# Kernel optimization log

Hardware: AMD Instinct MI355X
Metric: run time of the kernel (lower is better)

The kernel has to match this reference:

```python
import jax, jax.numpy as jnp
import numpy as np

N_NODES = 50000
N_EDGES = 800000
DIMS = [100, 512, 256, 128, 200]  # input -> conv1 -> conv2 -> conv3 -> conv4


def setup_inputs() -> dict:
    key = jax.random.key(0)
    ks = jax.random.split(key, 2 + 4)
    x = jax.random.normal(ks[0], (N_NODES, DIMS[0]), dtype=jnp.float32)
    edge_index = jax.random.randint(ks[1], (2, N_EDGES), 0, N_NODES, dtype=jnp.int64)
    inp = {"x": x, "edge_index": edge_index}
    for i in range(4):
        fan_in = DIMS[i]
        W = jax.random.normal(ks[2 + i], (DIMS[i], DIMS[i + 1]), dtype=jnp.float32) * (1.0 / np.sqrt(fan_in)).astype(np.float32)
        b = jnp.zeros((DIMS[i + 1],), dtype=jnp.float32)
        inp[f"W{i + 1}"] = W
        inp[f"b{i + 1}"] = b
    return inp


def _gcn_layer(x, row, col, norm, W, b, n):
    # PyG GCNConv: linear transform first, then normalized scatter-add, then bias.
    h = x @ W                           # [N, out]
    msg = h[row] * norm[:, None]        # [E+N, out] gather + edge scale
    agg = jax.ops.segment_sum(msg, col, num_segments=n)  # scatter-add to targets
    return agg + b


def reference(x, edge_index, W1, b1, W2, b2, W3, b3, W4, b4):
    n = x.shape[0]
    loop = jnp.arange(n, dtype=edge_index.dtype)
    row = jnp.concatenate([edge_index[0], loop])  # sources (with self-loops)
    col = jnp.concatenate([edge_index[1], loop])  # targets (with self-loops)
    deg = jax.ops.segment_sum(jnp.ones_like(col, dtype=x.dtype), col, num_segments=n)
    dinv = jnp.where(deg > 0, jax.lax.rsqrt(deg), 0.0)
    norm = dinv[row] * dinv[col]  # symmetric D^{-1/2}(A+I)D^{-1/2} edge weights

    out = jax.nn.relu(_gcn_layer(x, row, col, norm, W1, b1, n))
    out = jax.nn.relu(_gcn_layer(out, row, col, norm, W2, b2, n))
    out = jax.nn.relu(_gcn_layer(out, row, col, norm, W3, b3, n))
    out = jax.nn.relu(_gcn_layer(out, row, col, norm, W4, b4, n))
    return jnp.mean(out, axis=0, keepdims=True)  # [1, 200]
```

## Files before the change

kernel.cpp:

```cpp
#include <hip/hip_runtime.h>
#include <hip/hip_bf16.h>


#define NN 50000
#define NE 800000
#define NPART 8
#define PRANGE (NN / NPART)

typedef __attribute__((ext_vector_type(8))) _Float16 f16x8;
typedef __attribute__((ext_vector_type(4))) float floatx4;
typedef __attribute__((ext_vector_type(2))) float floatx2;

union U16x8 {
    uint4 u4;
    f16x8 h;
    _Float16 e[8];
};

__device__ __forceinline__ void dec16(const unsigned char* p, float* f) {
    uint4 v = *(const uint4*)p;
    unsigned w[4] = {v.x, v.y, v.z, v.w};
#pragma unroll
    for (int k = 0; k < 4; k++) {
        floatx2 lo = __builtin_amdgcn_cvt_pk_f32_fp8(w[k], false);
        floatx2 hi = __builtin_amdgcn_cvt_pk_f32_fp8(w[k], true);
        f[k * 4 + 0] = lo[0];
        f[k * 4 + 1] = lo[1];
        f[k * 4 + 2] = hi[0];
        f[k * 4 + 3] = hi[1];
    }
}

__device__ __forceinline__ uint4 enc16(const float* f) {
    uint4 r;
    unsigned w;
    w = __builtin_amdgcn_cvt_pk_fp8_f32(f[0], f[1], 0, false);
    w = __builtin_amdgcn_cvt_pk_fp8_f32(f[2], f[3], (int)w, true);
    r.x = w;
    w = __builtin_amdgcn_cvt_pk_fp8_f32(f[4], f[5], 0, false);
    w = __builtin_amdgcn_cvt_pk_fp8_f32(f[6], f[7], (int)w, true);
    r.y = w;
    w = __builtin_amdgcn_cvt_pk_fp8_f32(f[8], f[9], 0, false);
    w = __builtin_amdgcn_cvt_pk_fp8_f32(f[10], f[11], (int)w, true);
    r.z = w;
    w = __builtin_amdgcn_cvt_pk_fp8_f32(f[12], f[13], 0, false);
    w = __builtin_amdgcn_cvt_pk_fp8_f32(f[14], f[15], (int)w, true);
    r.w = w;
    return r;
}

__device__ __forceinline__ uint4 dec8_f16(uint2 v) {
    floatx2 f0 = __builtin_amdgcn_cvt_pk_f32_fp8(v.x, false);
    floatx2 f1 = __builtin_amdgcn_cvt_pk_f32_fp8(v.x, true);
    floatx2 f2 = __builtin_amdgcn_cvt_pk_f32_fp8(v.y, false);
    floatx2 f3 = __builtin_amdgcn_cvt_pk_f32_fp8(v.y, true);
    U16x8 o;
    o.e[0] = (_Float16)f0[0]; o.e[1] = (_Float16)f0[1];
    o.e[2] = (_Float16)f1[0]; o.e[3] = (_Float16)f1[1];
    o.e[4] = (_Float16)f2[0]; o.e[5] = (_Float16)f2[1];
    o.e[6] = (_Float16)f3[0]; o.e[7] = (_Float16)f3[1];
    return o.u4;
}

__global__ __launch_bounds__(256) void zero_detect_kernel(
    const unsigned* __restrict__ ei, int* __restrict__ flag,
    unsigned* __restrict__ cnt, unsigned* __restrict__ fillc,
    float* __restrict__ out) {
    int tid = blockIdx.x * 256 + threadIdx.x;
    if (tid < NN) {
        cnt[tid] = 0u;
        fillc[tid] = 0u;
    }
    if (blockIdx.x == 0) {
        if (threadIdx.x < 200) out[threadIdx.x] = 0.f;
        unsigned w = ei[2 * threadIdx.x + 1];
        unsigned long long any = __ballot(w != 0);
        if (threadIdx.x == 0) *flag = (any == 0ull) ? 1 : 0;
    }
}

__global__ __launch_bounds__(256) void count_kernel(const void* ei,
                                                    const int* __restrict__ flag,
                                                    unsigned* __restrict__ cnt) {
    const int part = blockIdx.x & 7;
    const int lo = part * PRANGE, hi = lo + PRANGE;
    const int group = blockIdx.x >> 3;
    const int f64 = *flag;
    const long long* p64 = (const long long*)ei + NE;
    const int* p32 = (const int*)ei + NE;
    for (int e = group * 256 + threadIdx.x; e < NE; e += 128 * 256) {
        int c = f64 ? (int)p64[e] : p32[e];
        if (c >= lo && c < hi) atomicAdd(&cnt[c], 1u);
    }
}

__global__ __launch_bounds__(256) void scan1_kernel(const unsigned* __restrict__ cnt,
                                                    int* __restrict__ off,
                                                    int* __restrict__ bsum,
                                                    float* __restrict__ dinv) {
    __shared__ int ws[4];
    int b = blockIdx.x, t = threadIdx.x;
    int base = b * 1024 + t * 4;
    int v[4];
    int s = 0;
#pragma unroll
    for (int i = 0; i < 4; i++) {
        int val = 0;
        if (base + i < NN) {
            val = (int)cnt[base + i];
            dinv[base + i] = rsqrtf((float)(val + 1));
        }
        v[i] = s;
        s += val;
    }
    int lane = t & 63, wv = t >> 6;
    int x = s;
    for (int d = 1; d < 64; d <<= 1) {
        int y = __shfl_up(x, d, 64);
        if (lane >= d) x += y;
    }
    if (lane == 63) ws[wv] = x;
    __syncthreads();
    int wpre = 0;
#pragma unroll
    for (int i = 0; i < 4; i++)
        if (i < wv) wpre += ws[i];
    int texcl = x - s + wpre;
#pragma unroll
    for (int i = 0; i < 4; i++)
        if (base + i < NN) off[base + i] = texcl + v[i];
    if (t == 255) bsum[b] = texcl + s;
}

__global__ void scan2_kernel(int* bsum, int nb) {
    int t = threadIdx.x;
    int v = (t < nb) ? bsum[t] : 0;
    int x = v;
    for (int d = 1; d < 64; d <<= 1) {
        int y = __shfl_up(x, d, 64);
        if (t >= d) x += y;
    }
    if (t < nb) bsum[t] = x - v;
}

__global__ __launch_bounds__(256) void scan3_kernel(int* __restrict__ off,
                                                    const int* __restrict__ bsum) {
    int b = blockIdx.x;
    int add = bsum[b];
    int base = b * 1024 + threadIdx.x * 4;
#pragma unroll
    for (int i = 0; i < 4; i++)
        if (base + i < NN) off[base + i] += add;
    if (b == 0 && threadIdx.x == 0) off[NN] = NE;
}

__global__ __launch_bounds__(256) void fill_kernel(
    const void* ei, const int* __restrict__ flag, const int* __restrict__ off,
    unsigned* __restrict__ fillc, int* __restrict__ ep) {
    const int part = blockIdx.x & 7;
    const int lo = part * PRANGE, hi = lo + PRANGE;
    const int group = blockIdx.x >> 3;
    const int f64 = *flag;
    const long long* p64 = (const long long*)ei;
    const int* p32 = (const int*)ei;
    for (int e = group * 256 + threadIdx.x; e < NE; e += 128 * 256) {
        int c = f64 ? (int)p64[NE + e] : p32[NE + e];
        if (c >= lo && c < hi) {
            int r = f64 ? (int)p64[e] : p32[e];
            int pos = off[c] + (int)atomicAdd(&fillc[c], 1u);
            ep[pos] = r;
        }
    }
}

__global__ __launch_bounds__(256) void xwcast_kernel(
    const float* __restrict__ x, unsigned char* __restrict__ xb,
    const float* __restrict__ W1, const float* __restrict__ W2,
    const float* __restrict__ W3, const float* __restrict__ W4,
    _Float16* __restrict__ w1t, _Float16* __restrict__ w2t,
    _Float16* __restrict__ w3t, _Float16* __restrict__ w4t) {
    int bx = blockIdx.x, t = threadIdx.x;
    if (bx < 1563) {
        int tid = bx * 256 + t;
        int node = tid >> 3, sub = tid & 7;
        if (node >= NN) return;
        int base = sub * 16;
        float f[16];
#pragma unroll
        for (int i = 0; i < 16; i++) {
            int c = base + i;
            f[i] = (c < 100) ? x[(size_t)node * 100 + c] : 0.f;
        }
        *(uint4*)(xb + (size_t)node * 128 + base) = enc16(f);
        return;
    }
    int b = bx - 1563;
    const float* W;
    _Float16* Wt;
    int K, N, Kpad, tid;
    if (b < 256)      { W = W1; Wt = w1t; K = 100; N = 512; Kpad = 128; tid = b * 256 + t; }
    else if (b < 768) { W = W2; Wt = w2t; K = 512; N = 256; Kpad = 512; tid = (b - 256) * 256 + t; }
    else if (b < 896) { W = W3; Wt = w3t; K = 256; N = 128; Kpad = 256; tid = (b - 768) * 256 + t; }
    else              { W = W4; Wt = w4t; K = 128; N = 200; Kpad = 128; tid = (b - 896) * 256 + t; }
    int n = tid / Kpad, k = tid - n * Kpad;
    float v = (k < K && n < N) ? W[(size_t)k * N + n] : 0.f;
    Wt[tid] = (_Float16)v;
}

template <int D, int BR>
__global__ __launch_bounds__(256) void agg_kernel(
    const unsigned char* __restrict__ H, const int* __restrict__ off,
    const int* __restrict__ ep, const float* __restrict__ dinv,
    const float* __restrict__ bias, unsigned char* __restrict__ O) {
    constexpr int LPN = D / 16;
    int tid = blockIdx.x * 256 + threadIdx.x;
    int node = tid / LPN;
    int sub = tid % LPN;
    if (node >= NN) return;
    int s = off[node], e = off[node + 1];
    float dc = dinv[node];
    float selfw = dc * dc;
    const int base = sub * 16;
    const unsigned char* __restrict__ Hb = H + base;
    float acc[16], t0[16], t1[16];
    dec16(Hb + (size_t)node * D, t0);
#pragma unroll
    for (int i = 0; i < 16; i++) acc[i] = selfw * t0[i];
    int j = s;
    for (; j + 2 <= e; j += 2) {
        int r0 = ep[j];
        int r1 = ep[j + 1];
        float w0 = dinv[r0] * dc;
        float w1 = dinv[r1] * dc;
        dec16(Hb + (size_t)r0 * D, t0);
        dec16(Hb + (size_t)r1 * D, t1);
#pragma unroll
        for (int i = 0; i < 16; i++) acc[i] = fmaf(w0, t0[i], acc[i]);
#pragma unroll
        for (int i = 0; i < 16; i++) acc[i] = fmaf(w1, t1[i], acc[i]);
    }
    if (j < e) {
        int r0 = ep[j];
        float w0 = dinv[r0] * dc;
        dec16(Hb + (size_t)r0 * D, t0);
#pragma unroll
        for (int i = 0; i < 16; i++) acc[i] = fmaf(w0, t0[i], acc[i]);
    }
    if (BR) {
#pragma unroll
        for (int i = 0; i < 16; i++) acc[i] = fmaxf(acc[i] + bias[base + i], 0.f);
    }
    *(uint4*)(O + (size_t)node * D + base) = enc16(acc);
}

template <int EPI>
__global__ __launch_bounds__(256) void gemm_kernel(
    const unsigned char* __restrict__ A, const _Float16* __restrict__ B,
    const float* __restrict__ bias, unsigned char* __restrict__ Cb,
    float* __restrict__ outmean, int M, int K, int N) {
    __shared__ _Float16 Asl[128 * 40];
    __shared__ _Float16 Bsl[128 * 40];
    __shared__ float red[128];
    const int m0 = blockIdx.y * 128;
    const int n0 = blockIdx.x * 128;
    const int t = threadIdx.x;
    const int lane = t & 63, w = t >> 6;
    const int wm = (w >> 1) * 64, wn = (w & 1) * 64;
    const int r16 = lane & 15, quad = lane >> 4;

    floatx4 acc[4][4];
    const floatx4 fz = {0.f, 0.f, 0.f, 0.f};
#pragma unroll
    for (int i = 0; i < 4; i++)
#pragma unroll
        for (int j = 0; j < 4; j++) acc[i][j] = fz;

    for (int kc = 0; kc < K; kc += 32) {
        __syncthreads();
#pragma unroll
        for (int i = 0; i < 2; i++) {
            int seg = t + 256 * i;
            int row = seg >> 2, k8 = (seg & 3) * 8;
            int gm = m0 + row;
            if (gm > M - 1) gm = M - 1;
            uint2 av = *(const uint2*)(A + (size_t)gm * K + kc + k8);
            *(uint4*)(Asl + row * 40 + k8) = dec8_f16(av);
            int gn = n0 + row;
            *(uint4*)(Bsl + row * 40 + k8) = *(const uint4*)(B + (size_t)gn * K + kc + k8);
        }
        __syncthreads();
        f16x8 af[4], bf[4];
#pragma unroll
        for (int i = 0; i < 4; i++)
            af[i] = *(const f16x8*)(Asl + (wm + i * 16 + r16) * 40 + quad * 8);
#pragma unroll
        for (int j = 0; j < 4; j++)
            bf[j] = *(const f16x8*)(Bsl + (wn + j * 16 + r16) * 40 + quad * 8);
#pragma unroll
        for (int i = 0; i < 4; i++)
#pragma unroll
            for (int j = 0; j < 4; j++)
                acc[i][j] = __builtin_amdgcn_mfma_f32_16x16x32_f16(af[i], bf[j], acc[i][j], 0, 0, 0);
    }

    if (EPI == 2) {
        if (t < 128) red[t] = 0.f;
        __syncthreads();
#pragma unroll
        for (int j = 0; j < 4; j++) {
            int col = n0 + wn + j * 16 + r16;
            float s = 0.f;
            if (col < N) {
                float bv = bias[col];
#pragma unroll
                for (int i = 0; i < 4; i++)
#pragma unroll
                    for (int r = 0; r < 4; r++) {
                        int m = m0 + wm + i * 16 + quad * 4 + r;
                        if (m < M) s += fmaxf(acc[i][j][r] + bv, 0.f);
                    }
            }
            atomicAdd(&red[wn + j * 16 + r16], s);
        }
        __syncthreads();
        if (t < 128) {
            int col = n0 + t;
            if (col < N) atomicAdd(outmean + col, red[t] * (1.0f / (float)NN));
        }
    } else {
#pragma unroll
        for (int i = 0; i < 4; i++)
#pragma unroll
            for (int r = 0; r < 4; r++) {
                int m = m0 + wm + i * 16 + quad * 4 + r;
                if (m >= M) continue;
#pragma unroll
                for (int j = 0; j < 4; j++) {
                    int col = n0 + wn + j * 16 + r16;
                    float v = acc[i][j][r];
                    if (EPI == 1) v = fmaxf(v + bias[col], 0.f);
                    unsigned pk = __builtin_amdgcn_cvt_pk_fp8_f32(v, v, 0, false);
                    Cb[(size_t)m * N + col] = (unsigned char)(pk & 0xffu);
                }
            }
    }
}

extern "C" void kernel_launch(void* const* d_in, const int* in_sizes, int n_in,
                              void* d_out, int out_size, void* d_ws, size_t ws_size,
                              hipStream_t stream) {
    const float* x  = (const float*)d_in[0];
    const void*  ei = d_in[1];
    const float* W1 = (const float*)d_in[2];
    const float* b1 = (const float*)d_in[3];
    const float* W2 = (const float*)d_in[4];
    const float* b2 = (const float*)d_in[5];
    const float* W3 = (const float*)d_in[6];
    const float* b3 = (const float*)d_in[7];
    const float* W4 = (const float*)d_in[8];
    const float* b4 = (const float*)d_in[9];
    float* out = (float*)d_out;

    char* ws = (char*)d_ws;
    size_t o = 0;
    auto alloc = [&](size_t bytes) -> void* {
        void* p = ws + o;
        o += (bytes + 255) & ~(size_t)255;
        return p;
    };
    int*      flag  = (int*)alloc(4);
    unsigned* cnt   = (unsigned*)alloc((size_t)NN * 4);
    int*      off   = (int*)alloc((size_t)(NN + 1) * 4);
    unsigned* fillc = (unsigned*)alloc((size_t)NN * 4);
    float*    dinv  = (float*)alloc((size_t)NN * 4);
    int*      ep    = (int*)alloc((size_t)NE * 4);
    _Float16* w1t = (_Float16*)alloc((size_t)512 * 128 * 2);
    _Float16* w2t = (_Float16*)alloc((size_t)256 * 512 * 2);
    _Float16* w3t = (_Float16*)alloc((size_t)128 * 256 * 2);
    _Float16* w4t = (_Float16*)alloc((size_t)256 * 128 * 2);
    int*      bsum  = (int*)alloc(256);
    unsigned char* xb  = (unsigned char*)alloc((size_t)NN * 128);
    unsigned char* A1b = (unsigned char*)alloc((size_t)NN * 128);
    unsigned char* H1b = (unsigned char*)alloc((size_t)NN * 512);
    unsigned char* t2b = (unsigned char*)alloc((size_t)NN * 256);
    unsigned char* H2b = (unsigned char*)alloc((size_t)NN * 256);
    unsigned char* t3b = (unsigned char*)alloc((size_t)NN * 128);
    unsigned char* h3b = (unsigned char*)alloc((size_t)NN * 128);
    unsigned char* A4b = (unsigned char*)alloc((size_t)NN * 128);

    const int NB1 = (NN + 1023) / 1024;
    const int ZB = (NN + 255) / 256;
    const int PB = 1024;

    zero_detect_kernel<<<ZB, 256, 0, stream>>>((const unsigned*)ei, flag, cnt, fillc, out);
    count_kernel<<<PB, 256, 0, stream>>>(ei, flag, cnt);
    scan1_kernel<<<NB1, 256, 0, stream>>>(cnt, off, bsum, dinv);
    scan2_kernel<<<1, 64, 0, stream>>>(bsum, NB1);
    scan3_kernel<<<NB1, 256, 0, stream>>>(off, bsum);
    fill_kernel<<<PB, 256, 0, stream>>>(ei, flag, off, fillc, ep);
    xwcast_kernel<<<1563 + 1024, 256, 0, stream>>>(x, xb, W1, W2, W3, W4, w1t, w2t, w3t, w4t);

    const int MB = (NN + 127) / 128;
    const int AB128 = (NN * 8 + 255) / 256;
    const int AB256 = (NN * 16 + 255) / 256;

    agg_kernel<128, 0><<<AB128, 256, 0, stream>>>(xb, off, ep, dinv, nullptr, A1b);
    gemm_kernel<1><<<dim3(4, MB), 256, 0, stream>>>(A1b, w1t, b1, H1b, nullptr, NN, 128, 512);
    gemm_kernel<0><<<dim3(2, MB), 256, 0, stream>>>(H1b, w2t, nullptr, t2b, nullptr, NN, 512, 256);
    agg_kernel<256, 1><<<AB256, 256, 0, stream>>>(t2b, off, ep, dinv, b2, H2b);
    gemm_kernel<0><<<dim3(1, MB), 256, 0, stream>>>(H2b, w3t, nullptr, t3b, nullptr, NN, 256, 128);
    agg_kernel<128, 1><<<AB128, 256, 0, stream>>>(t3b, off, ep, dinv, b3, h3b);
    agg_kernel<128, 0><<<AB128, 256, 0, stream>>>(h3b, off, ep, dinv, nullptr, A4b);
    gemm_kernel<2><<<dim3(2, MB), 256, 0, stream>>>(A4b, w4t, b4, nullptr, out, NN, 128, 200);
}
```

Before: 354.2 us.

## Halve GEMM M-tile, prefetch next K-chunk into registers, tighten LDS stride

The GEMM block tile shrinks from 128 to 64 rows, so each wave holds a 2x4 accumulator set and twice as many blocks launch. The next 32-wide K chunk of A and B is now loaded into registers while the current chunk's MFMAs run, so global latency overlaps compute. The LDS row stride drops from 40 to 36 halves, which changes bank mapping but leaves 128-bit LDS accesses only 8-byte aligned. The smaller tile means B is re-read by more blocks, and the alignment change could split or slow the shared-memory vector accesses.

```diff
diff --git a/kernel.cpp b/kernel.cpp
--- a/kernel.cpp
+++ b/kernel.cpp
@@ -258,46 +258,58 @@
     const unsigned char* __restrict__ A, const _Float16* __restrict__ B,
     const float* __restrict__ bias, unsigned char* __restrict__ Cb,
     float* __restrict__ outmean, int M, int K, int N) {
-    __shared__ _Float16 Asl[128 * 40];
-    __shared__ _Float16 Bsl[128 * 40];
+    __shared__ _Float16 Asl[64 * 36];
+    __shared__ _Float16 Bsl[128 * 36];
     __shared__ float red[128];
-    const int m0 = blockIdx.y * 128;
+    const int m0 = blockIdx.y * 64;
     const int n0 = blockIdx.x * 128;
     const int t = threadIdx.x;
     const int lane = t & 63, w = t >> 6;
-    const int wm = (w >> 1) * 64, wn = (w & 1) * 64;
+    const int wm = (w >> 1) * 32, wn = (w & 1) * 64;
     const int r16 = lane & 15, quad = lane >> 4;
 
-    floatx4 acc[4][4];
+    const int arow = t >> 2, ac8 = (t & 3) * 8;
+    int gma = m0 + arow; if (gma > M - 1) gma = M - 1;
+    const unsigned char* Aptr = A + (size_t)gma * K + ac8;
+    const int brow0 = t >> 1, bc8_0 = (t & 1) * 8;
+    const int brow1 = 128 + (t >> 1), bc8_1 = bc8_0;
+    const int cb0 = t, cb1 = t + 256;
+    const int rb0 = cb0 >> 2, kb0 = (cb0 & 3) * 8;
+    const int rb1 = cb1 >> 2, kb1 = (cb1 & 3) * 8;
+    const _Float16* Bptr0 = B + (size_t)(n0 + rb0) * K + kb0;
+    const _Float16* Bptr1 = B + (size_t)(n0 + rb1) * K + kb1;
+
+    floatx4 acc[2][4];
     const floatx4 fz = {0.f, 0.f, 0.f, 0.f};
 #pragma unroll
-    for (int i = 0; i < 4; i++)
+    for (int i = 0; i < 2; i++)
 #pragma unroll
         for (int j = 0; j < 4; j++) acc[i][j] = fz;
+
+    uint2 apf = *(const uint2*)Aptr;
+    uint4 bpf0 = *(const uint4*)Bptr0;
+    uint4 bpf1 = *(const uint4*)Bptr1;
 
     for (int kc = 0; kc < K; kc += 32) {
         __syncthreads();
-#pragma unroll
-        for (int i = 0; i < 2; i++) {
-            int seg = t + 256 * i;
-            int row = seg >> 2, k8 = (seg & 3) * 8;
-            int gm = m0 + row;
-            if (gm > M - 1) gm = M - 1;
-            uint2 av = *(const uint2*)(A + (size_t)gm * K + kc + k8);
-            *(uint4*)(Asl + row * 40 + k8) = dec8_f16(av);
-            int gn = n0 + row;
-            *(uint4*)(Bsl + row * 40 + k8) = *(const uint4*)(B + (size_t)gn * K + kc + k8);
-        }
+        *(uint4*)(Asl + arow * 36 + ac8) = dec8_f16(apf);
+        *(uint4*)(Bsl + rb0 * 36 + kb0) = bpf0;
+        *(uint4*)(Bsl + rb1 * 36 + kb1) = bpf1;
         __syncthreads();
-        f16x8 af[4], bf[4];
-#pragma unroll
-        for (int i = 0; i < 4; i++)
-            af[i] = *(const f16x8*)(Asl + (wm + i * 16 + r16) * 40 + quad * 8);
+        if (kc + 32 < K) {
+            apf = *(const uint2*)(Aptr + kc + 32);
+            bpf0 = *(const uint4*)(Bptr0 + kc + 32);
+            bpf1 = *(const uint4*)(Bptr1 + kc + 32);
+        }
+        f16x8 af[2], bf[4];
+#pragma unroll
+        for (int i = 0; i < 2; i++)
+            af[i] = *(const f16x8*)(Asl + (wm + i * 16 + r16) * 36 + quad * 8);
 #pragma unroll
         for (int j = 0; j < 4; j++)
-            bf[j] = *(const f16x8*)(Bsl + (wn + j * 16 + r16) * 40 + quad * 8);
-#pragma unroll
-        for (int i = 0; i < 4; i++)
+            bf[j] = *(const f16x8*)(Bsl + (wn + j * 16 + r16) * 36 + quad * 8);
+#pragma unroll
+        for (int i = 0; i < 2; i++)
 #pragma unroll
             for (int j = 0; j < 4; j++)
                 acc[i][j] = __builtin_amdgcn_mfma_f32_16x16x32_f16(af[i], bf[j], acc[i][j], 0, 0, 0);
@@ -313,12 +325,12 @@
             if (col < N) {
                 float bv = bias[col];
 #pragma unroll
-                for (int i = 0; i < 4; i++)
-#pragma unroll
-                    for (int r = 0; r < 4; r++) {
-                        int m = m0 + wm + i * 16 + quad * 4 + r;
-                        if (m < M) s += fmaxf(acc[i][j][r] + bv, 0.f);
-                    }
+                for (int i = 0; i < 2; i++) {
+                    int mbase = m0 + wm + i * 16 + quad * 4;
+#pragma unroll
+                    for (int r = 0; r < 4; r++)
+                        if (mbase + r < M) s += fmaxf(acc[i][j][r] + bv, 0.f);
+                }
             }
             atomicAdd(&red[wn + j * 16 + r16], s);
         }
@@ -329,10 +341,11 @@
         }
     } else {
 #pragma unroll
-        for (int i = 0; i < 4; i++)
+        for (int i = 0; i < 2; i++) {
+            int mbase = m0 + wm + i * 16 + quad * 4;
 #pragma unroll
             for (int r = 0; r < 4; r++) {
-                int m = m0 + wm + i * 16 + quad * 4 + r;
+                int m = mbase + r;
                 if (m >= M) continue;
 #pragma unroll
                 for (int j = 0; j < 4; j++) {
@@ -343,6 +356,7 @@
                     Cb[(size_t)m * N + col] = (unsigned char)(pk & 0xffu);
                 }
             }
+        }
     }
 }
 
@@ -400,16 +414,16 @@
     fill_kernel<<<PB, 256, 0, stream>>>(ei, flag, off, fillc, ep);
     xwcast_kernel<<<1563 + 1024, 256, 0, stream>>>(x, xb, W1, W2, W3, W4, w1t, w2t, w3t, w4t);
 
-    const int MB = (NN + 127) / 128;
+    const int MB64 = (NN + 63) / 64;
     const int AB128 = (NN * 8 + 255) / 256;
     const int AB256 = (NN * 16 + 255) / 256;
 
     agg_kernel<128, 0><<<AB128, 256, 0, stream>>>(xb, off, ep, dinv, nullptr, A1b);
-    gemm_kernel<1><<<dim3(4, MB), 256, 0, stream>>>(A1b, w1t, b1, H1b, nullptr, NN, 128, 512);
-    gemm_kernel<0><<<dim3(2, MB), 256, 0, stream>>>(H1b, w2t, nullptr, t2b, nullptr, NN, 512, 256);
+    gemm_kernel<1><<<dim3(4, MB64), 256, 0, stream>>>(A1b, w1t, b1, H1b, nullptr, NN, 128, 512);
+    gemm_kernel<0><<<dim3(2, MB64), 256, 0, stream>>>(H1b, w2t, nullptr, t2b, nullptr, NN, 512, 256);
     agg_kernel<256, 1><<<AB256, 256, 0, stream>>>(t2b, off, ep, dinv, b2, H2b);
-    gemm_kernel<0><<<dim3(1, MB), 256, 0, stream>>>(H2b, w3t, nullptr, t3b, nullptr, NN, 256, 128);
+    gemm_kernel<0><<<dim3(1, MB64), 256, 0, stream>>>(H2b, w3t, nullptr, t3b, nullptr, NN, 256, 128);
     agg_kernel<128, 1><<<AB128, 256, 0, stream>>>(t3b, off, ep, dinv, b3, h3b);
     agg_kernel<128, 0><<<AB128, 256, 0, stream>>>(h3b, off, ep, dinv, nullptr, A4b);
-    gemm_kernel<2><<<dim3(2, MB), 256, 0, stream>>>(A4b, w4t, b4, nullptr, out, NN, 128, 200);
-}
+    gemm_kernel<2><<<dim3(2, MB64), 256, 0, stream>>>(A4b, w4t, b4, nullptr, out, NN, 128, 200);
+}
```

Result: no change. 351.1 us (-0.9%).
